# Performance work log

Hardware: AMD Instinct MI355X
Metric: run time of the kernel (lower is better)

## Reference

```python
import jax, jax.numpy as jnp
import numpy as np

GRID_SIZE = 5
SPLINE_ORDER = 3
HIDDEN = 128
N = 131072
K = 256          # num_cluster
EPS = 1e-8       # torch.cosine_similarity eps
N_COEF = GRID_SIZE + SPLINE_ORDER  # 8 spline basis functions per input feature


def make_grid():
    # efficient-kan grid: grid_range [-1,1], extended by spline_order on each side
    h = 2.0 / GRID_SIZE
    g = jnp.arange(-SPLINE_ORDER, GRID_SIZE + SPLINE_ORDER + 1, dtype=jnp.float32) * h - 1.0
    return jnp.tile(g[None, :], (HIDDEN, 1))  # (in, grid_size + 2*order + 1) = (128, 12)


def b_splines(x, grid):
    # x: (N, in), grid: (in, G) -> bases: (N, in, grid_size + spline_order)
    xe = x[..., None]
    bases = ((xe >= grid[:, :-1]) & (xe < grid[:, 1:])).astype(x.dtype)
    for p in range(1, SPLINE_ORDER + 1):
        left = (xe - grid[:, :-(p + 1)]) / (grid[:, p:-1] - grid[:, :-(p + 1)])
        right = (grid[:, p + 1:] - xe) / (grid[:, p + 1:] - grid[:, 1:-p])
        bases = left * bases[..., :-1] + right * bases[..., 1:]
    return bases


def kan_linear(x, grid, base_w, spline_w, scaler):
    # efficient-kan KANLinear: base path + spline path
    base = jax.nn.silu(x) @ base_w.T                       # (N, out)
    sp = b_splines(x, grid)                                # (N, in, coef)
    sw = spline_w * scaler[..., None]                      # (out, in, coef)
    return base + jnp.einsum('nic,oic->no', sp, sw)


def setup_inputs() -> dict:
    key = jax.random.key(0)
    ks = jax.random.split(key, 9)
    s = 1.0 / np.sqrt(HIDDEN)
    return {
        'x': jax.random.normal(ks[0], (N, HIDDEN), jnp.float32),
        'prototypes': jax.random.normal(ks[1], (K, HIDDEN), jnp.float32),
        'grid': make_grid(),
        'base_w1': jax.random.normal(ks[2], (HIDDEN, HIDDEN), jnp.float32) * s,
        'spline_w1': jax.random.normal(ks[3], (HIDDEN, HIDDEN, N_COEF), jnp.float32) * 0.1,
        'scaler1': jax.random.normal(ks[4], (HIDDEN, HIDDEN), jnp.float32) * s + 1.0,
        'base_w2': jax.random.normal(ks[5], (HIDDEN, HIDDEN), jnp.float32) * s,
        'spline_w2': jax.random.normal(ks[6], (HIDDEN, HIDDEN, N_COEF), jnp.float32) * 0.1,
        'scaler2': jax.random.normal(ks[7], (HIDDEN, HIDDEN), jnp.float32) * s + 1.0,
    }


def reference(x, prototypes, grid, base_w1, spline_w1, scaler1, base_w2, spline_w2, scaler2):
    # KAN([128,128,128]) = two KANLinear layers
    h = kan_linear(x, grid, base_w1, spline_w1, scaler1)
    emb = kan_linear(h, grid, base_w2, spline_w2, scaler2)     # (N, 128)
    # cosine similarity to all prototypes = normalized matmul (same math as
    # the broadcasted torch.cosine_similarity, without the (N,K,H) intermediate)
    xn = emb / jnp.maximum(jnp.linalg.norm(emb, axis=-1, keepdims=True), EPS)
    pn = prototypes / jnp.maximum(jnp.linalg.norm(prototypes, axis=-1, keepdims=True), EPS)
    sim = xn @ pn.T                                            # (N, K)
    cluster_assignments = jnp.argmax(sim, axis=1)              # (N,)
    return emb, cluster_assignments
```

## Files before the change

kernel.cpp:

```cpp
#include <hip/hip_runtime.h>
#include <math.h>

typedef unsigned short u16;
typedef _Float16 f16;
typedef __attribute__((ext_vector_type(8))) _Float16 f16x8;
typedef __attribute__((ext_vector_type(4))) float f32x4;

#define N_ROWS 131072
#define HID 128
#define WS_CH 8192
#define N_WCH 72
#define N_PCH 8

__device__ __forceinline__ void f16_split(float v, f16& hi, f16& lo) {
    f16 h = (f16)v;
    hi = h;
    lo = (f16)(v - (float)h);
}

__device__ __forceinline__ void spline8(float xv, float* a8) {
    float s  = (xv + 2.2f) * 2.5f;
    float tf = floorf(s);
    int   tt = (int)tf;
    bool valid = (tt >= 0) && (tt <= 10);
    float kt = (float)(tt - 3) * 0.4f - 1.0f;
    float u  = (xv - kt) * 2.5f;
    float u2 = u * u, u3 = u2 * u;
    float om = 1.0f - u;
    float b3 = u3 * (1.0f / 6.0f);
    float b2 = (-3.f * u3 + 3.f * u2 + 3.f * u + 1.f) * (1.0f / 6.0f);
    float b1 = (3.f * u3 - 6.f * u2 + 4.f) * (1.0f / 6.0f);
    float b0 = om * om * om * (1.0f / 6.0f);
    #pragma unroll
    for (int c = 0; c < 8; ++c) {
        int d = tt - c;
        float v = 0.f;
        v = (d == 0) ? b3 : v;
        v = (d == 1) ? b2 : v;
        v = (d == 2) ? b1 : v;
        v = (d == 3) ? b0 : v;
        a8[c] = valid ? v : 0.f;
    }
}

__global__ __launch_bounds__(256)
void pack_weights(const float* __restrict__ bw1, const float* __restrict__ sw1,
                  const float* __restrict__ sc1,
                  const float* __restrict__ bw2, const float* __restrict__ sw2,
                  const float* __restrict__ sc2,
                  const float* __restrict__ protos, u16* __restrict__ ws)
{
    int gid = blockIdx.x * 256 + threadIdx.x;
    if (gid < N_WCH * 4096) {
        int l  = gid / (36 * 4096);
        int r  = gid % (36 * 4096);
        int ch = r / 4096;
        int e  = r % 4096;
        int o  = e >> 5;
        int kl = e & 31;
        const float* bw = l ? bw2 : bw1;
        const float* sw = l ? sw2 : sw1;
        const float* sc = l ? sc2 : sc1;
        float v;
        if (ch < 4) {
            v = bw[o * HID + ch * 32 + kl];
        } else {
            int i = (ch - 4) * 4 + (kl >> 3);
            v = sw[(o * HID + i) * 8 + (kl & 7)] * sc[o * HID + i];
        }
        f16 hi, lo; f16_split(v, hi, lo);
        int nt = o >> 4, n = o & 15, kq = kl >> 3, c = kl & 7;
        size_t base = (size_t)(l * 36 + ch) * WS_CH;
        size_t idx  = ((size_t)nt * 64 + kq * 16 + n) * 8 + c;
        ws[base + idx]        = __builtin_bit_cast(u16, hi);
        ws[base + 4096 + idx] = __builtin_bit_cast(u16, lo);
    } else if (gid < (N_WCH + N_PCH) * 4096) {
        int r  = gid - N_WCH * 4096;
        int hk = r / 4096;
        int e  = r % 4096;
        int pl = e >> 5;
        int kl = e & 31;
        int half = hk >> 2, kc = hk & 3;
        float v = protos[(size_t)(half * 128 + pl) * HID + kc * 32 + kl];
        f16 hi, lo; f16_split(v, hi, lo);
        int nt = pl >> 4, n = pl & 15, kq = kl >> 3, c = kl & 7;
        size_t base = (size_t)(N_WCH + hk) * WS_CH;
        size_t idx  = ((size_t)nt * 64 + kq * 16 + n) * 8 + c;
        ws[base + idx]        = __builtin_bit_cast(u16, hi);
        ws[base + 4096 + idx] = __builtin_bit_cast(u16, lo);
    }
}

__global__ __launch_bounds__(256, 3)
void kan_fused(const float* __restrict__ x, const float* __restrict__ protos,
               const u16* __restrict__ wpack,
               float* __restrict__ emb_out, float* __restrict__ assign_out)
{
    __shared__ float t[64][132];
    __shared__ u16   Bfrag[2][8][64][8];
    __shared__ float rnp[256];

    const int tid  = threadIdx.x;
    const int lane = tid & 63;
    const int w    = tid >> 6;
    const int m    = lane & 15;
    const int q    = lane >> 4;
    const int row  = w * 16 + m;
    const int brow = blockIdx.x * 64;
    const int woff = w * 256 + lane;

    uint4 rr0, rr1, rr2, rr3;

#define ISSUE_LOADS(region) do {                                                   \
        const uint4* _g = (const uint4*)(wpack + (size_t)(region) * WS_CH) + woff; \
        rr0 = _g[0]; rr1 = _g[64]; rr2 = _g[128]; rr3 = _g[192];                   \
    } while (0)

#define STORE_LDS() do {                                                           \
        uint4* _l = (uint4*)&Bfrag[0][0][0][0] + woff;                             \
        _l[0] = rr0; _l[64] = rr1; _l[128] = rr2; _l[192] = rr3;                   \
    } while (0)

#define PIPE_BARRIER() do {                                                        \
        asm volatile("s_waitcnt lgkmcnt(0)" ::: "memory");                         \
        __builtin_amdgcn_s_barrier();                                              \
        __builtin_amdgcn_sched_barrier(0);                                         \
    } while (0)

    ISSUE_LOADS(0);

    {
        const float4* pr = (const float4*)(protos + (size_t)tid * HID);
        float s = 0.0f;
        #pragma unroll
        for (int j = 0; j < 32; ++j) {
            float4 v = pr[j];
            s += v.x * v.x + v.y * v.y + v.z * v.z + v.w * v.w;
        }
        rnp[tid] = 1.0f / fmaxf(sqrtf(s), 1e-8f);
    }

    {
        const int m2 = tid >> 2, kq2 = tid & 3;
        const float4* src = (const float4*)(x + (size_t)(brow + m2) * HID + kq2 * 32);
        #pragma unroll
        for (int j = 0; j < 8; ++j) {
            float4 v = src[j];
            int k = kq2 * 32 + j * 4;
            t[m2][k] = v.x; t[m2][k + 1] = v.y; t[m2][k + 2] = v.z; t[m2][k + 3] = v.w;
        }
    }
    PIPE_BARRIER();

    union { f16x8 v; f16 h[8]; } ah, al, bh, bl;
    f32x4 acc[8];

    for (int l = 0; l < 2; ++l) {
        #pragma unroll
        for (int nt = 0; nt < 8; ++nt) acc[nt] = (f32x4){0.f, 0.f, 0.f, 0.f};

        for (int ch = 0; ch < 36; ++ch) {
            float a8[8];
            if (ch < 4) {
                const float4* tr = (const float4*)&t[row][ch * 32 + q * 8];
                float4 v0 = tr[0], v1 = tr[1];
                float xs[8] = {v0.x, v0.y, v0.z, v0.w, v1.x, v1.y, v1.z, v1.w};
                #pragma unroll
                for (int j = 0; j < 8; ++j)
                    a8[j] = xs[j] * __builtin_amdgcn_rcpf(1.0f + __expf(-xs[j]));
            } else {
                spline8(t[row][(ch - 4) * 4 + q], a8);
            }
            #pragma unroll
            for (int j = 0; j < 8; ++j) f16_split(a8[j], ah.h[j], al.h[j]);

            PIPE_BARRIER();
            STORE_LDS();
            ISSUE_LOADS(l * 36 + ch + 1);
            PIPE_BARRIER();

            #pragma unroll
            for (int nt = 0; nt < 8; ++nt) {
                bh.v = *(const f16x8*)Bfrag[0][nt][lane];
                bl.v = *(const f16x8*)Bfrag[1][nt][lane];
                acc[nt] = __builtin_amdgcn_mfma_f32_16x16x32_f16(ah.v, bh.v, acc[nt], 0, 0, 0);
                acc[nt] = __builtin_amdgcn_mfma_f32_16x16x32_f16(al.v, bh.v, acc[nt], 0, 0, 0);
                acc[nt] = __builtin_amdgcn_mfma_f32_16x16x32_f16(ah.v, bl.v, acc[nt], 0, 0, 0);
            }
        }

        #pragma unroll
        for (int nt = 0; nt < 8; ++nt)
            #pragma unroll
            for (int r = 0; r < 4; ++r)
                t[w * 16 + q * 4 + r][nt * 16 + m] = acc[nt][r];
    }

    PIPE_BARRIER();

    {
        const int m2 = tid >> 2, kq2 = tid & 3;
        float* dst = emb_out + (size_t)(brow + m2) * HID + kq2 * 32;
        #pragma unroll
        for (int j = 0; j < 8; ++j)
            *(float4*)(dst + j * 4) = *(const float4*)&t[m2][kq2 * 32 + j * 4];
    }

    float best[4]; int bi[4];
    #pragma unroll
    for (int r = 0; r < 4; ++r) { best[r] = -3.402823466e+38f; bi[r] = 0; }

    for (int half = 0; half < 2; ++half) {
        #pragma unroll
        for (int nt = 0; nt < 8; ++nt) acc[nt] = (f32x4){0.f, 0.f, 0.f, 0.f};

        for (int kc = 0; kc < 4; ++kc) {
            float a8[8];
            {
                const float4* tr = (const float4*)&t[row][kc * 32 + q * 8];
                float4 v0 = tr[0], v1 = tr[1];
                a8[0] = v0.x; a8[1] = v0.y; a8[2] = v0.z; a8[3] = v0.w;
                a8[4] = v1.x; a8[5] = v1.y; a8[6] = v1.z; a8[7] = v1.w;
            }
            #pragma unroll
            for (int j = 0; j < 8; ++j) f16_split(a8[j], ah.h[j], al.h[j]);

            PIPE_BARRIER();
            STORE_LDS();
            {
                int nxt = 72 + half * 4 + kc + 1;
                ISSUE_LOADS(nxt > 79 ? 79 : nxt);
            }
            PIPE_BARRIER();

            #pragma unroll
            for (int nt = 0; nt < 8; ++nt) {
                bh.v = *(const f16x8*)Bfrag[0][nt][lane];
                bl.v = *(const f16x8*)Bfrag[1][nt][lane];
                acc[nt] = __builtin_amdgcn_mfma_f32_16x16x32_f16(ah.v, bh.v, acc[nt], 0, 0, 0);
                acc[nt] = __builtin_amdgcn_mfma_f32_16x16x32_f16(al.v, bh.v, acc[nt], 0, 0, 0);
                acc[nt] = __builtin_amdgcn_mfma_f32_16x16x32_f16(ah.v, bl.v, acc[nt], 0, 0, 0);
            }
        }

        #pragma unroll
        for (int nt = 0; nt < 8; ++nt) {
            int p = half * 128 + nt * 16 + m;
            float rp = rnp[p];
            #pragma unroll
            for (int r = 0; r < 4; ++r) {
                float v = acc[nt][r] * rp;
                if (v > best[r]) { best[r] = v; bi[r] = p; }
            }
        }
    }

    #pragma unroll
    for (int r = 0; r < 4; ++r) {
        #pragma unroll
        for (int off = 1; off < 16; off <<= 1) {
            float ov = __shfl_xor(best[r], off);
            int   oi = __shfl_xor(bi[r], off);
            if (ov > best[r] || (ov == best[r] && oi < bi[r])) { best[r] = ov; bi[r] = oi; }
        }
        if (m == 0)
            assign_out[(size_t)brow + w * 16 + q * 4 + r] = (float)bi[r];
    }
}

extern "C" void kernel_launch(void* const* d_in, const int* in_sizes, int n_in,
                              void* d_out, int out_size, void* d_ws, size_t ws_size,
                              hipStream_t stream) {
    (void)in_sizes; (void)n_in; (void)out_size; (void)ws_size;

    const float* x      = (const float*)d_in[0];
    const float* protos = (const float*)d_in[1];
    const float* bw1 = (const float*)d_in[3];
    const float* sw1 = (const float*)d_in[4];
    const float* sc1 = (const float*)d_in[5];
    const float* bw2 = (const float*)d_in[6];
    const float* sw2 = (const float*)d_in[7];
    const float* sc2 = (const float*)d_in[8];

    float* out    = (float*)d_out;
    float* embp   = out;
    float* assign = out + (size_t)N_ROWS * HID;
    u16*   wpack  = (u16*)d_ws;

    pack_weights<<<dim3((N_WCH + N_PCH) * 4096 / 256), dim3(256), 0, stream>>>(
        bw1, sw1, sc1, bw2, sw2, sc2, protos, wpack);
    kan_fused<<<dim3(N_ROWS / 64), dim3(256), 0, stream>>>(
        x, protos, wpack, embp, assign);
}
```

Baseline: 425.1 us.

## Double-buffer weight staging via direct global-to-LDS loads and prenormalize prototypes

Weight chunks now go straight from global memory into LDS using global_load_lds into a double-buffered fragment array, so each chunk's fetch overlaps the previous chunk's MFMA work and costs one barrier per chunk instead of two. The activation tile drops its padding and uses an XOR swizzle to avoid bank conflicts. Prototype normalization moves into the packing kernel, which removes the per-block norm computation and the rnp table. The larger LDS footprint lowers launch bounds from 3 to 2 blocks per SM, which may reduce occupancy.

```diff
diff --git a/kernel.cpp b/kernel.cpp
--- a/kernel.cpp
+++ b/kernel.cpp
@@ -41,6 +41,15 @@
         v = (d == 3) ? b0 : v;
         a8[c] = valid ? v : 0.f;
     }
+}
+
+#define GLOAD_LDS16(g, l)                                                         \
+    __builtin_amdgcn_global_load_lds(                                             \
+        (const __attribute__((address_space(1))) unsigned int*)(g),               \
+        (__attribute__((address_space(3))) unsigned int*)(l), 16, 0, 0)
+
+__device__ __forceinline__ int tswz(int r, int c) {
+    return (r << 7) + ((((c >> 2) ^ r) & 31) << 2) + (c & 3);
 }
 
 __global__ __launch_bounds__(256)
@@ -81,7 +90,13 @@
         int pl = e >> 5;
         int kl = e & 31;
         int half = hk >> 2, kc = hk & 3;
-        float v = protos[(size_t)(half * 128 + pl) * HID + kc * 32 + kl];
+        int p = half * 128 + pl;
+        const float4 pv = *(const float4*)(protos + (size_t)p * HID + kl * 4);
+        float s = pv.x * pv.x + pv.y * pv.y + pv.z * pv.z + pv.w * pv.w;
+        #pragma unroll
+        for (int off = 1; off < 32; off <<= 1) s += __shfl_xor(s, off);
+        float rp = 1.0f / fmaxf(sqrtf(s), 1e-8f);
+        float v = protos[(size_t)p * HID + kc * 32 + kl] * rp;
         f16 hi, lo; f16_split(v, hi, lo);
         int nt = pl >> 4, n = pl & 15, kq = kl >> 3, c = kl & 7;
         size_t base = (size_t)(N_WCH + hk) * WS_CH;
@@ -91,14 +106,12 @@
     }
 }
 
-__global__ __launch_bounds__(256, 3)
-void kan_fused(const float* __restrict__ x, const float* __restrict__ protos,
-               const u16* __restrict__ wpack,
+__global__ __launch_bounds__(256, 2)
+void kan_fused(const float* __restrict__ x, const u16* __restrict__ wpack,
                float* __restrict__ emb_out, float* __restrict__ assign_out)
 {
-    __shared__ float t[64][132];
-    __shared__ u16   Bfrag[2][8][64][8];
-    __shared__ float rnp[256];
+    __shared__ float t[64 * 128];
+    __shared__ u16   Bfrag[2][2][8][64][8];
 
     const int tid  = threadIdx.x;
     const int lane = tid & 63;
@@ -107,38 +120,24 @@
     const int q    = lane >> 4;
     const int row  = w * 16 + m;
     const int brow = blockIdx.x * 64;
-    const int woff = w * 256 + lane;
-
-    uint4 rr0, rr1, rr2, rr3;
-
-#define ISSUE_LOADS(region) do {                                                   \
-        const uint4* _g = (const uint4*)(wpack + (size_t)(region) * WS_CH) + woff; \
-        rr0 = _g[0]; rr1 = _g[64]; rr2 = _g[128]; rr3 = _g[192];                   \
+
+#define STAGE(reg_, buf_) do {                                                     \
+        const char* _g = (const char*)(wpack + (size_t)(reg_) * WS_CH)             \
+                         + w * 4096 + (size_t)lane * 16;                           \
+        char* _l = (char*)&Bfrag[(buf_)][0][0][0][0] + w * 4096;                   \
+        GLOAD_LDS16(_g,        _l);                                                \
+        GLOAD_LDS16(_g + 1024, _l + 1024);                                         \
+        GLOAD_LDS16(_g + 2048, _l + 2048);                                         \
+        GLOAD_LDS16(_g + 3072, _l + 3072);                                         \
     } while (0)
 
-#define STORE_LDS() do {                                                           \
-        uint4* _l = (uint4*)&Bfrag[0][0][0][0] + woff;                             \
-        _l[0] = rr0; _l[64] = rr1; _l[128] = rr2; _l[192] = rr3;                   \
-    } while (0)
-
-#define PIPE_BARRIER() do {                                                        \
-        asm volatile("s_waitcnt lgkmcnt(0)" ::: "memory");                         \
+#define CHUNK_BARRIER() do {                                                       \
+        asm volatile("s_waitcnt vmcnt(0)" ::: "memory");                           \
         __builtin_amdgcn_s_barrier();                                              \
         __builtin_amdgcn_sched_barrier(0);                                         \
     } while (0)
 
-    ISSUE_LOADS(0);
-
-    {
-        const float4* pr = (const float4*)(protos + (size_t)tid * HID);
-        float s = 0.0f;
-        #pragma unroll
-        for (int j = 0; j < 32; ++j) {
-            float4 v = pr[j];
-            s += v.x * v.x + v.y * v.y + v.z * v.z + v.w * v.w;
-        }
-        rnp[tid] = 1.0f / fmaxf(sqrtf(s), 1e-8f);
-    }
+    STAGE(0, 0);
 
     {
         const int m2 = tid >> 2, kq2 = tid & 3;
@@ -146,11 +145,10 @@
         #pragma unroll
         for (int j = 0; j < 8; ++j) {
             float4 v = src[j];
-            int k = kq2 * 32 + j * 4;
-            t[m2][k] = v.x; t[m2][k + 1] = v.y; t[m2][k + 2] = v.z; t[m2][k + 3] = v.w;
-        }
-    }
-    PIPE_BARRIER();
+            *(float4*)&t[tswz(m2, kq2 * 32 + j * 4)] = v;
+        }
+    }
+    CHUNK_BARRIER();
 
     union { f16x8 v; f16 h[8]; } ah, al, bh, bl;
     f32x4 acc[8];
@@ -160,50 +158,48 @@
         for (int nt = 0; nt < 8; ++nt) acc[nt] = (f32x4){0.f, 0.f, 0.f, 0.f};
 
         for (int ch = 0; ch < 36; ++ch) {
+            const int reg = l * 36 + ch;
+            const int cur = reg & 1;
+            STAGE(reg + 1, cur ^ 1);
+
             float a8[8];
             if (ch < 4) {
-                const float4* tr = (const float4*)&t[row][ch * 32 + q * 8];
-                float4 v0 = tr[0], v1 = tr[1];
+                float4 v0 = *(const float4*)&t[tswz(row, ch * 32 + q * 8)];
+                float4 v1 = *(const float4*)&t[tswz(row, ch * 32 + q * 8 + 4)];
                 float xs[8] = {v0.x, v0.y, v0.z, v0.w, v1.x, v1.y, v1.z, v1.w};
                 #pragma unroll
                 for (int j = 0; j < 8; ++j)
                     a8[j] = xs[j] * __builtin_amdgcn_rcpf(1.0f + __expf(-xs[j]));
             } else {
-                spline8(t[row][(ch - 4) * 4 + q], a8);
+                spline8(t[tswz(row, (ch - 4) * 4 + q)], a8);
             }
             #pragma unroll
             for (int j = 0; j < 8; ++j) f16_split(a8[j], ah.h[j], al.h[j]);
 
-            PIPE_BARRIER();
-            STORE_LDS();
-            ISSUE_LOADS(l * 36 + ch + 1);
-            PIPE_BARRIER();
-
             #pragma unroll
             for (int nt = 0; nt < 8; ++nt) {
-                bh.v = *(const f16x8*)Bfrag[0][nt][lane];
-                bl.v = *(const f16x8*)Bfrag[1][nt][lane];
+                bh.v = *(const f16x8*)Bfrag[cur][0][nt][lane];
+                bl.v = *(const f16x8*)Bfrag[cur][1][nt][lane];
                 acc[nt] = __builtin_amdgcn_mfma_f32_16x16x32_f16(ah.v, bh.v, acc[nt], 0, 0, 0);
                 acc[nt] = __builtin_amdgcn_mfma_f32_16x16x32_f16(al.v, bh.v, acc[nt], 0, 0, 0);
                 acc[nt] = __builtin_amdgcn_mfma_f32_16x16x32_f16(ah.v, bl.v, acc[nt], 0, 0, 0);
             }
+            CHUNK_BARRIER();
         }
 
         #pragma unroll
         for (int nt = 0; nt < 8; ++nt)
             #pragma unroll
             for (int r = 0; r < 4; ++r)
-                t[w * 16 + q * 4 + r][nt * 16 + m] = acc[nt][r];
-    }
-
-    PIPE_BARRIER();
+                t[tswz(w * 16 + q * 4 + r, nt * 16 + m)] = acc[nt][r];
+    }
 
     {
         const int m2 = tid >> 2, kq2 = tid & 3;
         float* dst = emb_out + (size_t)(brow + m2) * HID + kq2 * 32;
         #pragma unroll
         for (int j = 0; j < 8; ++j)
-            *(float4*)(dst + j * 4) = *(const float4*)&t[m2][kq2 * 32 + j * 4];
+            *(float4*)(dst + j * 4) = *(const float4*)&t[tswz(m2, kq2 * 32 + j * 4)];
     }
 
     float best[4]; int bi[4];
@@ -215,41 +211,37 @@
         for (int nt = 0; nt < 8; ++nt) acc[nt] = (f32x4){0.f, 0.f, 0.f, 0.f};
 
         for (int kc = 0; kc < 4; ++kc) {
+            const int reg = N_WCH + half * 4 + kc;
+            const int cur = reg & 1;
+            if (reg != 79) STAGE(reg + 1, cur ^ 1);
+
             float a8[8];
             {
-                const float4* tr = (const float4*)&t[row][kc * 32 + q * 8];
-                float4 v0 = tr[0], v1 = tr[1];
+                float4 v0 = *(const float4*)&t[tswz(row, kc * 32 + q * 8)];
+                float4 v1 = *(const float4*)&t[tswz(row, kc * 32 + q * 8 + 4)];
                 a8[0] = v0.x; a8[1] = v0.y; a8[2] = v0.z; a8[3] = v0.w;
                 a8[4] = v1.x; a8[5] = v1.y; a8[6] = v1.z; a8[7] = v1.w;
             }
             #pragma unroll
             for (int j = 0; j < 8; ++j) f16_split(a8[j], ah.h[j], al.h[j]);
 
-            PIPE_BARRIER();
-            STORE_LDS();
-            {
-                int nxt = 72 + half * 4 + kc + 1;
-                ISSUE_LOADS(nxt > 79 ? 79 : nxt);
-            }
-            PIPE_BARRIER();
-
             #pragma unroll
             for (int nt = 0; nt < 8; ++nt) {
-                bh.v = *(const f16x8*)Bfrag[0][nt][lane];
-                bl.v = *(const f16x8*)Bfrag[1][nt][lane];
+                bh.v = *(const f16x8*)Bfrag[cur][0][nt][lane];
+                bl.v = *(const f16x8*)Bfrag[cur][1][nt][lane];
                 acc[nt] = __builtin_amdgcn_mfma_f32_16x16x32_f16(ah.v, bh.v, acc[nt], 0, 0, 0);
                 acc[nt] = __builtin_amdgcn_mfma_f32_16x16x32_f16(al.v, bh.v, acc[nt], 0, 0, 0);
                 acc[nt] = __builtin_amdgcn_mfma_f32_16x16x32_f16(ah.v, bl.v, acc[nt], 0, 0, 0);
             }
+            CHUNK_BARRIER();
         }
 
         #pragma unroll
         for (int nt = 0; nt < 8; ++nt) {
             int p = half * 128 + nt * 16 + m;
-            float rp = rnp[p];
             #pragma unroll
             for (int r = 0; r < 4; ++r) {
-                float v = acc[nt][r] * rp;
+                float v = acc[nt][r];
                 if (v > best[r]) { best[r] = v; bi[r] = p; }
             }
         }
@@ -266,6 +258,8 @@
         if (m == 0)
             assign_out[(size_t)brow + w * 16 + q * 4 + r] = (float)bi[r];
     }
+#undef STAGE
+#undef CHUNK_BARRIER
 }
 
 extern "C" void kernel_launch(void* const* d_in, const int* in_sizes, int n_in,
@@ -290,5 +284,5 @@
     pack_weights<<<dim3((N_WCH + N_PCH) * 4096 / 256), dim3(256), 0, stream>>>(
         bw1, sw1, sc1, bw2, sw2, sc2, protos, wpack);
     kan_fused<<<dim3(N_ROWS / 64), dim3(256), 0, stream>>>(
-        x, protos, wpack, embp, assign);
-}
+        x, wpack, embp, assign);
+}
```

Measured after the change: 434.0 us. 1.02x slower.
